# Kernel tuning notes

Hardware: AMD Instinct MI355X
Metric: run time of the kernel (lower is better)

Reference implementation:

```python
import jax, jax.numpy as jnp
import numpy as np

B, C, W, H = 8, 256, 64, 64
DQK = C // 8  # 32


def setup_inputs() -> dict:
    key = jax.random.key(0)
    ks = jax.random.split(key, 5)
    x = jax.random.normal(ks[0], (B, C, W, H), dtype=jnp.float32)
    # 1x1 conv weights as [out_ch, in_ch]; scaled ~ spectral-normalized magnitude
    w_q = jax.random.normal(ks[1], (DQK, C), dtype=jnp.float32) * (1.0 / np.sqrt(C))
    w_k = jax.random.normal(ks[2], (DQK, C), dtype=jnp.float32) * (1.0 / np.sqrt(C))
    w_v = jax.random.normal(ks[3], (C, C), dtype=jnp.float32) * (1.0 / np.sqrt(C))
    b_q = jnp.zeros((DQK,), dtype=jnp.float32)
    b_k = jnp.zeros((DQK,), dtype=jnp.float32)
    b_v = jnp.zeros((C,), dtype=jnp.float32)
    gamma = jax.random.normal(ks[4], (1,), dtype=jnp.float32)
    return {"x": x, "w_q": w_q, "b_q": b_q, "w_k": w_k, "b_k": b_k,
            "w_v": w_v, "b_v": b_v, "gamma": gamma}


def reference(x, w_q, b_q, w_k, b_k, w_v, b_v, gamma):
    b, c, w, h = x.shape
    n = w * h
    xf = x.reshape(b, c, n)  # [B, C, N]
    # 1x1 convs == channel-mixing matmuls
    q = jnp.einsum('dc,bcn->bnd', w_q, xf) + b_q  # [B, N, Dqk]
    k = jnp.einsum('dc,bcn->bdn', w_k, xf) + b_k[None, :, None]  # [B, Dqk, N]
    v = jnp.einsum('oc,bcn->bon', w_v, xf) + b_v[None, :, None]  # [B, C, N]
    energy = jnp.einsum('bnd,bdm->bnm', q, k)  # [B, N, N]
    attn = jax.nn.softmax(energy, axis=-1)
    # out[b,c,i] = sum_j v[b,c,j] * attn[b,i,j]  (bmm(v, attn^T))
    out = jnp.einsum('bcj,bij->bci', v, attn).reshape(b, c, w, h)
    return gamma[0] * out + x
```

## Files before the change

kernel.cpp:

```cpp
#include <hip/hip_runtime.h>
#include <hip/hip_bf16.h>

typedef __attribute__((ext_vector_type(8))) short short8;
typedef __attribute__((ext_vector_type(4))) float f32x4;
typedef __attribute__((ext_vector_type(16))) float f32x16;

#define NB 8
#define NC 256
#define NN 4096
#define ND 32
#define NCH 16
#define LOG2E 1.44269504088896340736f

#define PIDX(row, col) (((row) << 8) + ((col) ^ (((row) & 15) << 3)))

static __device__ __forceinline__ ushort f2bf(float f) {
  __hip_bfloat16 h = __float2bfloat16(f);
  return reinterpret_cast<ushort&>(h);
}
static __device__ __forceinline__ float bf2f(ushort u) {
  const uint v = ((uint)u) << 16;
  return __builtin_bit_cast(float, v);
}

#define LDW 264
#define LDX 40
#define LDO 136

__global__ __launch_bounds__(256, 2)
void proj_kernel(const float* __restrict__ x,
                 const float* __restrict__ wq, const float* __restrict__ bq,
                 const float* __restrict__ wk, const float* __restrict__ bk,
                 const float* __restrict__ wv, const float* __restrict__ bv,
                 ushort* __restrict__ qk, ushort* __restrict__ vt) {
  __shared__ __align__(16) ushort Ws[2][64 * LDW];
  __shared__ __align__(16) ushort Xs[128 * LDX];

  const int n0 = blockIdx.x * 128;
  const int o0 = blockIdx.y * 64;
  const int b  = blockIdx.z;
  const int t  = threadIdx.x;
  const int w  = t >> 6;
  const int lane = t & 63;
  const int g16  = lane >> 4;
  const int c16  = lane & 15;

  {
    const int o  = t >> 2;
    const int cb = (t & 3) * 64;
    const int oa = o0 + o;
    const float* wrow;
    float scale = 1.0f;
    if (oa < 32)       { wrow = wq + (size_t)oa * NC; scale = LOG2E; }
    else if (oa < 64)  { wrow = wk + (size_t)(oa - 32) * NC; }
    else               { wrow = wv + (size_t)(oa - 64) * NC; }
#pragma unroll
    for (int cc = 0; cc < 64; cc += 8) {
      const float4 f0 = *(const float4*)(wrow + cb + cc);
      const float4 f1 = *(const float4*)(wrow + cb + cc + 4);
      float v[8] = {f0.x, f0.y, f0.z, f0.w, f1.x, f1.y, f1.z, f1.w};
      union { ushort u[8]; uint4 q; } hi, lo;
#pragma unroll
      for (int e = 0; e < 8; ++e) {
        const float s = v[e] * scale;
        const ushort h = f2bf(s);
        hi.u[e] = h;
        lo.u[e] = f2bf(s - bf2f(h));
      }
      *(uint4*)&Ws[0][o * LDW + cb + cc] = hi.q;
      *(uint4*)&Ws[1][o * LDW + cb + cc] = lo.q;
    }
  }

  f32x4 acc[8];
#pragma unroll
  for (int nt = 0; nt < 8; ++nt)
#pragma unroll
    for (int r = 0; r < 4; ++r) acc[nt][r] = 0.f;

  const int s_cc = w * 8 + (lane >> 3);
  const int s_nb = (lane & 7) * 4;

  for (int c0 = 0; c0 < NC; c0 += 32) {
    __syncthreads();
    {
      const float* xsrc = x + ((size_t)(b * NC + c0 + s_cc)) * NN + n0 + s_nb;
#pragma unroll
      for (int it = 0; it < 4; ++it) {
        const float4 f = *(const float4*)(xsrc + it * 32);
        const int n = s_nb + it * 32;
        Xs[(n + 0) * LDX + s_cc] = f2bf(f.x);
        Xs[(n + 1) * LDX + s_cc] = f2bf(f.y);
        Xs[(n + 2) * LDX + s_cc] = f2bf(f.z);
        Xs[(n + 3) * LDX + s_cc] = f2bf(f.w);
      }
    }
    __syncthreads();

    const short8 ah = *(const short8*)&Ws[0][(w * 16 + c16) * LDW + c0 + g16 * 8];
    const short8 al = *(const short8*)&Ws[1][(w * 16 + c16) * LDW + c0 + g16 * 8];
#pragma unroll
    for (int nt = 0; nt < 8; ++nt) {
      const short8 bf = *(const short8*)&Xs[(nt * 16 + c16) * LDX + g16 * 8];
      acc[nt] = __builtin_amdgcn_mfma_f32_16x16x32_bf16(ah, bf, acc[nt], 0, 0, 0);
      acc[nt] = __builtin_amdgcn_mfma_f32_16x16x32_bf16(al, bf, acc[nt], 0, 0, 0);
    }
  }

  if (blockIdx.y == 0) {
    float bb[4];
#pragma unroll
    for (int r = 0; r < 4; ++r) {
      const int o = w * 16 + g16 * 4 + r;
      bb[r] = (o < 32) ? bq[o] * LOG2E : bk[o - 32];
    }
#pragma unroll
    for (int nt = 0; nt < 8; ++nt) {
      union { ushort u[4]; uint2 v; } pk;
#pragma unroll
      for (int r = 0; r < 4; ++r) pk.u[r] = f2bf(acc[nt][r] + bb[r]);
      const int n = n0 + nt * 16 + c16;
      *(uint2*)(qk + ((size_t)(b * NN + n)) * 64 + w * 16 + g16 * 4) = pk.v;
    }
  } else {
    const int ch0 = o0 - 64;
    float bb[4];
#pragma unroll
    for (int r = 0; r < 4; ++r) bb[r] = bv[ch0 + w * 16 + g16 * 4 + r];
    __syncthreads();
    ushort* Os = &Ws[0][0];
#pragma unroll
    for (int nt = 0; nt < 8; ++nt) {
#pragma unroll
      for (int r = 0; r < 4; ++r)
        Os[(w * 16 + g16 * 4 + r) * LDO + nt * 16 + c16] =
            f2bf(acc[nt][r] + bb[r]);
    }
    __syncthreads();
    const int chl = t >> 2;
    const int nb  = (t & 3) * 32;
    ushort* dst = vt + ((size_t)(b * NC + ch0 + chl)) * NN + n0 + nb;
#pragma unroll
    for (int k = 0; k < 4; ++k)
      *(uint4*)(dst + k * 8) = *(const uint4*)&Os[chl * LDO + nb + k * 8];
  }
}

__global__ __launch_bounds__(768, 3)
void attn_kernel(const ushort* __restrict__ qk, const ushort* __restrict__ vt,
                 const float* __restrict__ x, const float* __restrict__ gamma,
                 float* __restrict__ out) {
  __shared__ __align__(16) ushort P[2][128 * 256];
  __shared__ __align__(16) float lL[128];

  const int lin  = blockIdx.x;
  const int b    = lin & 7;
  const int i0   = (lin >> 3) * 128;
  const int t    = threadIdx.x;
  const int w    = t >> 6;
  const int lane = t & 63;
  const int g16  = lane >> 4;
  const int c16  = lane & 15;
  const int l5   = lane >> 5;
  const int c32  = lane & 31;

  const f32x4 zero = {0.f, 0.f, 0.f, 0.f};
  const bool isS = (w < 4);

  const int prow0 = w * 32 + c16;
  const int prow1 = prow0 + 16;
  short8 qf0, qf1;
  short8 kf[8];
  float lp0 = 0.f, lp1 = 0.f;
  const ushort* kbase = qk + ((size_t)b * NN) * 64 + 32 + g16 * 8;
  if (isS) {
    qf0 = *(const short8*)(qk + ((size_t)(b * NN + i0 + prow0)) * 64 + g16 * 8);
    qf1 = *(const short8*)(qk + ((size_t)(b * NN + i0 + prow1)) * 64 + g16 * 8);
  }

  const int p = w - 4;
  f32x16 OA[4];
  const ushort* vptr = nullptr;
  if (!isS) {
#pragma unroll
    for (int isub = 0; isub < 4; ++isub)
#pragma unroll
      for (int e = 0; e < 16; ++e) OA[isub][e] = 0.f;
    vptr = vt + ((size_t)(b * NC + p * 32 + c32)) * NN + l5 * 8;
  }

  for (int iv = 0; iv <= NCH; ++iv) {
    if (isS) {
      if (iv < NCH) {
        ushort* Pb = P[iv & 1];
        const ushort* kch = kbase + (size_t)iv * 256 * 64;
#pragma unroll
        for (int h = 0; h < 2; ++h) {
#pragma unroll
          for (int jt = 0; jt < 8; ++jt)
            kf[jt] = *(const short8*)(
                kch + (size_t)(h * 128 + jt * 16 + c16) * 64);
#pragma unroll
          for (int jt = 0; jt < 8; ++jt) {
            const f32x4 s0 = __builtin_amdgcn_mfma_f32_16x16x32_bf16(
                kf[jt], qf0, zero, 0, 0, 0);
            const f32x4 s1 = __builtin_amdgcn_mfma_f32_16x16x32_bf16(
                kf[jt], qf1, zero, 0, 0, 0);
            union { ushort u[4]; uint2 v; } pk0, pk1;
#pragma unroll
            for (int r = 0; r < 4; ++r) {
              const float e0 = exp2f(s0[r]);
              const float e1 = exp2f(s1[r]);
              lp0 += e0; lp1 += e1;
              pk0.u[r] = f2bf(e0); pk1.u[r] = f2bf(e1);
            }
            const int col = h * 128 + jt * 16 + g16 * 4;
            *(uint2*)&Pb[PIDX(prow0, col)] = pk0.v;
            *(uint2*)&Pb[PIDX(prow1, col)] = pk1.v;
          }
        }
      } else {
        lp0 += __shfl_xor(lp0, 16); lp0 += __shfl_xor(lp0, 32);
        lp1 += __shfl_xor(lp1, 16); lp1 += __shfl_xor(lp1, 32);
        if (g16 == 0) { lL[prow0] = lp0; lL[prow1] = lp1; }
      }
    } else if (iv >= 1) {
      const int ch = iv - 1;
      const ushort* Pb = P[ch & 1];
      const int j0 = ch * 256;
      short8 vf[2];
      vf[0] = *(const short8*)(vptr + j0);
      __builtin_amdgcn_s_setprio(1);
#pragma unroll
      for (int ji = 0; ji < 16; ++ji) {
        if (ji + 1 < 16)
          vf[(ji + 1) & 1] = *(const short8*)(vptr + j0 + (ji + 1) * 16);
        const int jo = ji * 16;
        const short8 v0 = vf[ji & 1];
#pragma unroll
        for (int isub = 0; isub < 4; ++isub) {
          const short8 pa =
              *(const short8*)&Pb[PIDX(isub * 32 + c32, jo + l5 * 8)];
          OA[isub] = __builtin_amdgcn_mfma_f32_32x32x16_bf16(
              pa, v0, OA[isub], 0, 0, 0);
        }
      }
      __builtin_amdgcn_s_setprio(0);
    }
    __syncthreads();
  }

  if (!isS) {
    const float g = gamma[0];
#pragma unroll
    for (int isub = 0; isub < 4; ++isub) {
#pragma unroll
      for (int q = 0; q < 4; ++q) {
        const int r0 = isub * 32 + q * 8 + l5 * 4;
        const f32x4 li = *(const f32x4*)&lL[r0];
        f32x4 gi;
#pragma unroll
        for (int r = 0; r < 4; ++r) gi[r] = g / li[r];
        const int c = p * 32 + c32;
        const size_t base = ((size_t)(b * NC + c)) * NN + i0 + r0;
        const f32x4 xv = *(const f32x4*)(x + base);
        f32x4 ov;
#pragma unroll
        for (int r = 0; r < 4; ++r) ov[r] = OA[isub][q * 4 + r] * gi[r] + xv[r];
        *(f32x4*)(out + base) = ov;
      }
    }
  }
}

extern "C" void kernel_launch(void* const* d_in, const int* in_sizes, int n_in,
                              void* d_out, int out_size, void* d_ws, size_t ws_size,
                              hipStream_t stream) {
  const float* x  = (const float*)d_in[0];
  const float* wq = (const float*)d_in[1];
  const float* bq = (const float*)d_in[2];
  const float* wk = (const float*)d_in[3];
  const float* bk = (const float*)d_in[4];
  const float* wv = (const float*)d_in[5];
  const float* bv = (const float*)d_in[6];
  const float* gm = (const float*)d_in[7];
  float* outp = (float*)d_out;

  ushort* qkw = (ushort*)d_ws;
  ushort* vtw = qkw + (size_t)NB * NN * 64;

  proj_kernel<<<dim3(NN / 128, 5, NB), 256, 0, stream>>>(
      x, wq, bq, wk, bk, wv, bv, qkw, vtw);
  attn_kernel<<<dim3((NN / 128) * NB), 768, 0, stream>>>(qkw, vtw, x, gm, outp);
}
```

Before: 151.7 us.

## Replace warp-specialised attention with per-wave fused score and PV tiles

Drops the producer/consumer split, in which score waves wrote a shared P buffer consumed by PV waves with block-wide barriers. Each of 4 waves now computes its own 64x64 exp-score tile into a private LDS slab and immediately multiplies it with V for 64 channels. Block-level synchronisation goes away and the K loads are prefetched one chunk ahead. In exchange, QK^T and exp are recomputed by all four waves for the same query rows, quadrupling score and exponent work.

New measurement: 250.2 us. 1.65x slower.

```diff
diff --git a/kernel.cpp b/kernel.cpp
--- a/kernel.cpp
+++ b/kernel.cpp
@@ -3,16 +3,12 @@
 
 typedef __attribute__((ext_vector_type(8))) short short8;
 typedef __attribute__((ext_vector_type(4))) float f32x4;
-typedef __attribute__((ext_vector_type(16))) float f32x16;
 
 #define NB 8
 #define NC 256
 #define NN 4096
 #define ND 32
-#define NCH 16
 #define LOG2E 1.44269504088896340736f
-
-#define PIDX(row, col) (((row) << 8) + ((col) ^ (((row) & 15) << 3)))
 
 static __device__ __forceinline__ ushort f2bf(float f) {
   __hip_bfloat16 h = __float2bfloat16(f);
@@ -146,129 +142,131 @@
   }
 }
 
-__global__ __launch_bounds__(768, 3)
+#define PX(r, c) (((r) << 6) + ((((c) & 56) ^ (((r) & 7) << 3)) | ((c) & 7)))
+
+__global__ __launch_bounds__(256, 2)
 void attn_kernel(const ushort* __restrict__ qk, const ushort* __restrict__ vt,
                  const float* __restrict__ x, const float* __restrict__ gamma,
                  float* __restrict__ out) {
-  __shared__ __align__(16) ushort P[2][128 * 256];
-  __shared__ __align__(16) float lL[128];
+  __shared__ __align__(16) ushort Pw[4][64 * 64];
+  __shared__ __align__(16) float lw[4][64];
 
   const int lin  = blockIdx.x;
   const int b    = lin & 7;
-  const int i0   = (lin >> 3) * 128;
+  const int i0   = (lin >> 3) * 64;
   const int t    = threadIdx.x;
   const int w    = t >> 6;
   const int lane = t & 63;
   const int g16  = lane >> 4;
   const int c16  = lane & 15;
-  const int l5   = lane >> 5;
-  const int c32  = lane & 31;
+  const int ch0  = w * 64;
 
   const f32x4 zero = {0.f, 0.f, 0.f, 0.f};
-  const bool isS = (w < 4);
-
-  const int prow0 = w * 32 + c16;
-  const int prow1 = prow0 + 16;
-  short8 qf0, qf1;
-  short8 kf[8];
-  float lp0 = 0.f, lp1 = 0.f;
+  ushort* Pp = &Pw[w][0];
+
+  short8 qf[4];
+#pragma unroll
+  for (int ig = 0; ig < 4; ++ig)
+    qf[ig] = *(const short8*)(
+        qk + ((size_t)(b * NN + i0 + ig * 16 + c16)) * 64 + g16 * 8);
+
   const ushort* kbase = qk + ((size_t)b * NN) * 64 + 32 + g16 * 8;
-  if (isS) {
-    qf0 = *(const short8*)(qk + ((size_t)(b * NN + i0 + prow0)) * 64 + g16 * 8);
-    qf1 = *(const short8*)(qk + ((size_t)(b * NN + i0 + prow1)) * 64 + g16 * 8);
-  }
-
-  const int p = w - 4;
-  f32x16 OA[4];
-  const ushort* vptr = nullptr;
-  if (!isS) {
-#pragma unroll
-    for (int isub = 0; isub < 4; ++isub)
-#pragma unroll
-      for (int e = 0; e < 16; ++e) OA[isub][e] = 0.f;
-    vptr = vt + ((size_t)(b * NC + p * 32 + c32)) * NN + l5 * 8;
-  }
-
-  for (int iv = 0; iv <= NCH; ++iv) {
-    if (isS) {
-      if (iv < NCH) {
-        ushort* Pb = P[iv & 1];
-        const ushort* kch = kbase + (size_t)iv * 256 * 64;
-#pragma unroll
-        for (int h = 0; h < 2; ++h) {
-#pragma unroll
-          for (int jt = 0; jt < 8; ++jt)
-            kf[jt] = *(const short8*)(
-                kch + (size_t)(h * 128 + jt * 16 + c16) * 64);
-#pragma unroll
-          for (int jt = 0; jt < 8; ++jt) {
-            const f32x4 s0 = __builtin_amdgcn_mfma_f32_16x16x32_bf16(
-                kf[jt], qf0, zero, 0, 0, 0);
-            const f32x4 s1 = __builtin_amdgcn_mfma_f32_16x16x32_bf16(
-                kf[jt], qf1, zero, 0, 0, 0);
-            union { ushort u[4]; uint2 v; } pk0, pk1;
-#pragma unroll
-            for (int r = 0; r < 4; ++r) {
-              const float e0 = exp2f(s0[r]);
-              const float e1 = exp2f(s1[r]);
-              lp0 += e0; lp1 += e1;
-              pk0.u[r] = f2bf(e0); pk1.u[r] = f2bf(e1);
-            }
-            const int col = h * 128 + jt * 16 + g16 * 4;
-            *(uint2*)&Pb[PIDX(prow0, col)] = pk0.v;
-            *(uint2*)&Pb[PIDX(prow1, col)] = pk1.v;
-          }
+  const ushort* vb[4];
+#pragma unroll
+  for (int cf = 0; cf < 4; ++cf)
+    vb[cf] = vt + ((size_t)(b * NC + ch0 + cf * 16 + c16)) * NN + g16 * 8;
+
+  f32x4 o[4][4];
+#pragma unroll
+  for (int ig = 0; ig < 4; ++ig)
+#pragma unroll
+    for (int cf = 0; cf < 4; ++cf)
+#pragma unroll
+      for (int r = 0; r < 4; ++r) o[ig][cf][r] = 0.f;
+
+  float lp[4] = {0.f, 0.f, 0.f, 0.f};
+
+  short8 kf[4], kfn[4];
+#pragma unroll
+  for (int kt = 0; kt < 4; ++kt)
+    kf[kt] = *(const short8*)(kbase + (size_t)(kt * 16 + c16) * 64);
+
+  for (int jc = 0; jc < NN / 64; ++jc) {
+    const int j0 = jc * 64;
+
+#pragma unroll
+    for (int ig = 0; ig < 4; ++ig) {
+#pragma unroll
+      for (int kt = 0; kt < 4; ++kt) {
+        const f32x4 d = __builtin_amdgcn_mfma_f32_16x16x32_bf16(
+            kf[kt], qf[ig], zero, 0, 0, 0);
+        union { ushort u[4]; uint2 v; } pk;
+#pragma unroll
+        for (int r = 0; r < 4; ++r) {
+          const float e = exp2f(d[r]);
+          lp[ig] += e;
+          pk.u[r] = f2bf(e);
         }
-      } else {
-        lp0 += __shfl_xor(lp0, 16); lp0 += __shfl_xor(lp0, 32);
-        lp1 += __shfl_xor(lp1, 16); lp1 += __shfl_xor(lp1, 32);
-        if (g16 == 0) { lL[prow0] = lp0; lL[prow1] = lp1; }
+        *(uint2*)&Pp[PX(ig * 16 + c16, kt * 16 + g16 * 4)] = pk.v;
       }
-    } else if (iv >= 1) {
-      const int ch = iv - 1;
-      const ushort* Pb = P[ch & 1];
-      const int j0 = ch * 256;
-      short8 vf[2];
-      vf[0] = *(const short8*)(vptr + j0);
-      __builtin_amdgcn_s_setprio(1);
-#pragma unroll
-      for (int ji = 0; ji < 16; ++ji) {
-        if (ji + 1 < 16)
-          vf[(ji + 1) & 1] = *(const short8*)(vptr + j0 + (ji + 1) * 16);
-        const int jo = ji * 16;
-        const short8 v0 = vf[ji & 1];
-#pragma unroll
-        for (int isub = 0; isub < 4; ++isub) {
-          const short8 pa =
-              *(const short8*)&Pb[PIDX(isub * 32 + c32, jo + l5 * 8)];
-          OA[isub] = __builtin_amdgcn_mfma_f32_32x32x16_bf16(
-              pa, v0, OA[isub], 0, 0, 0);
-        }
-      }
-      __builtin_amdgcn_s_setprio(0);
-    }
-    __syncthreads();
-  }
-
-  if (!isS) {
-    const float g = gamma[0];
-#pragma unroll
-    for (int isub = 0; isub < 4; ++isub) {
-#pragma unroll
-      for (int q = 0; q < 4; ++q) {
-        const int r0 = isub * 32 + q * 8 + l5 * 4;
-        const f32x4 li = *(const f32x4*)&lL[r0];
-        f32x4 gi;
-#pragma unroll
-        for (int r = 0; r < 4; ++r) gi[r] = g / li[r];
-        const int c = p * 32 + c32;
-        const size_t base = ((size_t)(b * NC + c)) * NN + i0 + r0;
-        const f32x4 xv = *(const f32x4*)(x + base);
-        f32x4 ov;
-#pragma unroll
-        for (int r = 0; r < 4; ++r) ov[r] = OA[isub][q * 4 + r] * gi[r] + xv[r];
-        *(f32x4*)(out + base) = ov;
-      }
+    }
+
+    if (jc + 1 < NN / 64) {
+#pragma unroll
+      for (int kt = 0; kt < 4; ++kt)
+        kfn[kt] = *(const short8*)(
+            kbase + (size_t)(j0 + 64 + kt * 16 + c16) * 64);
+    }
+
+#pragma unroll
+    for (int ks = 0; ks < 2; ++ks) {
+      short8 vf[4];
+#pragma unroll
+      for (int cf = 0; cf < 4; ++cf)
+        vf[cf] = *(const short8*)(vb[cf] + j0 + ks * 32);
+      short8 pa[4];
+#pragma unroll
+      for (int ig = 0; ig < 4; ++ig)
+        pa[ig] = *(const short8*)&Pp[PX(ig * 16 + c16, ks * 32 + g16 * 8)];
+#pragma unroll
+      for (int ig = 0; ig < 4; ++ig)
+#pragma unroll
+        for (int cf = 0; cf < 4; ++cf)
+          o[ig][cf] = __builtin_amdgcn_mfma_f32_16x16x32_bf16(
+              pa[ig], vf[cf], o[ig][cf], 0, 0, 0);
+    }
+
+#pragma unroll
+    for (int kt = 0; kt < 4; ++kt) kf[kt] = kfn[kt];
+  }
+
+#pragma unroll
+  for (int ig = 0; ig < 4; ++ig) {
+    lp[ig] += __shfl_xor(lp[ig], 16);
+    lp[ig] += __shfl_xor(lp[ig], 32);
+  }
+  if (g16 == 0) {
+#pragma unroll
+    for (int ig = 0; ig < 4; ++ig) lw[w][ig * 16 + c16] = lp[ig];
+  }
+
+  const float g = gamma[0];
+#pragma unroll
+  for (int ig = 0; ig < 4; ++ig) {
+    const f32x4 li = *(const f32x4*)&lw[w][ig * 16 + g16 * 4];
+    f32x4 gi;
+#pragma unroll
+    for (int r = 0; r < 4; ++r) gi[r] = g / li[r];
+    const int irow = i0 + ig * 16 + g16 * 4;
+#pragma unroll
+    for (int cf = 0; cf < 4; ++cf) {
+      const int c = ch0 + cf * 16 + c16;
+      const size_t base = ((size_t)(b * NC + c)) * NN + irow;
+      const f32x4 xv = *(const f32x4*)(x + base);
+      f32x4 ov;
+#pragma unroll
+      for (int r = 0; r < 4; ++r) ov[r] = o[ig][cf][r] * gi[r] + xv[r];
+      *(f32x4*)(out + base) = ov;
     }
   }
 }
@@ -291,5 +289,5 @@
 
   proj_kernel<<<dim3(NN / 128, 5, NB), 256, 0, stream>>>(
       x, wq, bq, wk, bk, wv, bv, qkw, vtw);
-  attn_kernel<<<dim3((NN / 128) * NB), 768, 0, stream>>>(qkw, vtw, x, gm, outp);
-}
+  attn_kernel<<<dim3((NN / 64) * NB), 256, 0, stream>>>(qkw, vtw, x, gm, outp);
+}
```
